# Performance work log

Hardware: AMD Instinct MI355X
Metric: run time of the kernel (lower is better)

The kernel has to match this reference:

```python
import jax, jax.numpy as jnp
import numpy as np

ND, NL, E, M = 8000, 16000, 60000, 50000  # disease nodes, lncrna nodes, edges, label edges
H = 16  # attention heads


def _gat(h_src, h_dst, src, dst, Ws, Wd, a_s, a_d, b, n_dst):
    # PyG GATConv: bipartite, concat heads, add_self_loops=False, negative_slope=0.2
    Hh, C = a_s.shape
    zs = (h_src @ Ws).reshape(-1, Hh, C)   # [Ns,H,C]
    zd = (h_dst @ Wd).reshape(-1, Hh, C)   # [Nd,H,C]
    al = (zs * a_s).sum(-1)[src] + (zd * a_d).sum(-1)[dst]  # [E,H]
    al = jax.nn.leaky_relu(al, negative_slope=0.2)
    m = jax.ops.segment_max(al, dst, num_segments=n_dst)
    m = jnp.where(jnp.isfinite(m), m, 0.0)  # guard empty segments
    e = jnp.exp(al - m[dst])
    s = jax.ops.segment_sum(e, dst, num_segments=n_dst)
    alpha = e / (s[dst] + 1e-16)            # softmax over incoming edges per dst
    msg = zs[src] * alpha[:, :, None]       # [E,H,C]
    out = jax.ops.segment_sum(msg, dst, num_segments=n_dst)
    return out.reshape(n_dst, Hh * C) + b


def _head_mean(x):
    x = jax.nn.relu(x)
    return x.reshape(x.shape[0], H, -1).mean(axis=1)


def _forward(x_d, x_l, emb_d, emb_l, lin_dw, lin_db, lin_lw, lin_lb,
             Wsrc1, Wdst1, asrc1, adst1, b1,
             Wsrc2, Wdst2, asrc2, adst2, b2,
             Wsrc3, Wdst3, asrc3, adst3, b3,
             pw, pb, fc1w, fc1b, fc2w, fc2b,
             node_id_d, node_id_l, edge_src, edge_dst, label_src, label_dst):
    hd = x_d @ lin_dw + lin_db + emb_d[node_id_d]   # [ND,128]
    hl = x_l @ lin_lw + lin_lb + emb_l[node_id_l]   # [NL,128]
    for (Ws, Wd, a_s, a_d, b) in ((Wsrc1, Wdst1, asrc1, adst1, b1),
                                  (Wsrc2, Wdst2, asrc2, adst2, b2),
                                  (Wsrc3, Wdst3, asrc3, adst3, b3)):
        # to_hetero: edge-type 0 = disease->lncrna (target lncrna); 1 = reverse
        out_l = _gat(hd, hl, edge_src, edge_dst, Ws[0], Wd[0], a_s[0], a_d[0], b[0], NL)
        out_d = _gat(hl, hd, edge_dst, edge_src, Ws[1], Wd[1], a_s[1], a_d[1], b[1], ND)
        hd, hl = _head_mean(out_d), _head_mean(out_l)
    # penalty scaling (per node type after to_hetero); transformer branch is dead code
    hd = hd * jnp.exp(hd @ pw[0] + pb[0])
    hl = hl * jnp.exp(hl @ pw[1] + pb[1])
    f = jnp.concatenate([hd[label_src], hl[label_dst]], axis=-1)  # [M,64]
    return jax.nn.relu(f @ fc1w + fc1b) @ fc2w + fc2b              # [M,1]


def setup_inputs():
    key = jax.random.key(0)
    ks = jax.random.split(key, 40)
    def rn(i, shape, scale=1.0):
        return jax.random.normal(ks[i], shape, dtype=jnp.float32) * scale
    return dict(
        x_d=rn(0, (ND, 412)), x_l=rn(1, (NL, 240)),
        node_id_d=jnp.arange(ND), node_id_l=jnp.arange(NL),
        edge_src=jax.random.randint(ks[2], (E,), 0, ND),
        edge_dst=jax.random.randint(ks[3], (E,), 0, NL),
        label_src=jax.random.randint(ks[4], (M,), 0, ND),
        label_dst=jax.random.randint(ks[5], (M,), 0, NL),
        emb_d=rn(6, (ND, 128), 0.1), emb_l=rn(7, (NL, 128), 0.1),
        lin_dw=rn(8, (412, 128), 412 ** -0.5), lin_db=rn(9, (128,), 0.02),
        lin_lw=rn(10, (240, 128), 240 ** -0.5), lin_lb=rn(11, (128,), 0.02),
        Wsrc1=rn(12, (2, 128, 2048), 128 ** -0.5), Wdst1=rn(13, (2, 128, 2048), 128 ** -0.5),
        asrc1=rn(14, (2, H, 128), 0.05), adst1=rn(15, (2, H, 128), 0.05), b1=rn(16, (2, 2048), 0.02),
        Wsrc2=rn(17, (2, 128, 2048), 128 ** -0.5), Wdst2=rn(18, (2, 128, 2048), 128 ** -0.5),
        asrc2=rn(19, (2, H, 128), 0.05), adst2=rn(20, (2, H, 128), 0.05), b2=rn(21, (2, 2048), 0.02),
        Wsrc3=rn(22, (2, 128, 512), 128 ** -0.5), Wdst3=rn(23, (2, 128, 512), 128 ** -0.5),
        asrc3=rn(24, (2, H, 32), 0.05), adst3=rn(25, (2, H, 32), 0.05), b3=rn(26, (2, 512), 0.02),
        pw=rn(27, (2, 32, 1), 0.05), pb=rn(28, (2, 1), 0.01),
        fc1w=rn(29, (64, 64), 64 ** -0.5), fc1b=rn(30, (64,), 0.02),
        fc2w=rn(31, (64, 1), 64 ** -0.5), fc2b=rn(32, (1,), 0.02),
    )


def reference(x_d, x_l, node_id_d, node_id_l, edge_src, edge_dst, label_src, label_dst,
              emb_d, emb_l, lin_dw, lin_db, lin_lw, lin_lb,
              Wsrc1, Wdst1, asrc1, adst1, b1,
              Wsrc2, Wdst2, asrc2, adst2, b2,
              Wsrc3, Wdst3, asrc3, adst3, b3,
              pw, pb, fc1w, fc1b, fc2w, fc2b):
    return _forward(x_d, x_l, emb_d, emb_l, lin_dw, lin_db, lin_lw, lin_lb,
                    Wsrc1, Wdst1, asrc1, adst1, b1,
                    Wsrc2, Wdst2, asrc2, adst2, b2,
                    Wsrc3, Wdst3, asrc3, adst3, b3,
                    pw, pb, fc1w, fc1b, fc2w, fc2b,
                    node_id_d, node_id_l, edge_src, edge_dst, label_src, label_dst)
```

## Files before the change

### kernel.cpp

```cpp
#include <hip/hip_runtime.h>
#include <cstdint>
#include <cstddef>

#define ND 8000
#define NL 16000
#define NE 60000
#define NM 50000

#define BM 64
#define BN 64
#define BK 16

typedef __attribute__((ext_vector_type(8))) short bf16x8;
typedef __attribute__((ext_vector_type(4))) float f32x4;
typedef __attribute__((ext_vector_type(8))) unsigned int u32x8;

__device__ __forceinline__ unsigned short f2bf(float x) {
    unsigned int u = __float_as_uint(x);
    unsigned int r = (u + 0x7FFFu + ((u >> 16) & 1u)) >> 16;
    return (unsigned short)r;
}
__device__ __forceinline__ float bf2f(unsigned short b) {
    return __uint_as_float(((unsigned int)b) << 16);
}
__device__ __forceinline__ float lrelu(float x) {
    return x >= 0.f ? x : 0.2f * x;
}

__device__ __forceinline__ void gl_lds16(const void* g, void* l) {
    __builtin_amdgcn_global_load_lds(
        (const __attribute__((address_space(1))) void*)g,
        (__attribute__((address_space(3))) void*)l, 16, 0, 0);
}

__global__ __launch_bounds__(256) void gemm3_kernel(
    const float* __restrict__ hd, const float* __restrict__ hl,
    const float* __restrict__ W,
    float* __restrict__ zs3d, float* __restrict__ zs3l)
{
    __shared__ float As[BK][BM + 4];
    __shared__ float Bs[BK][BN + 4];
    int mt = blockIdx.y;
    const float* A; const float* B; float* Cm;
    if (mt < 125) { A = hd; B = W; Cm = zs3d; }
    else { mt -= 125; A = hl; B = W + 128 * 512; Cm = zs3l; }
    const int tid = threadIdx.x;
    const int tx = tid & 15, ty = tid >> 4;
    const int bm = mt * BM, bn = blockIdx.x * BN;
    float acc[4][4] = {};
    for (int k0 = 0; k0 < 128; k0 += BK) {
#pragma unroll
        for (int i = 0; i < 4; ++i) {
            int idx = tid + i * 256;
            int ml = idx >> 4, kl = idx & 15;
            As[kl][ml] = A[(size_t)(bm + ml) * 128 + k0 + kl];
        }
#pragma unroll
        for (int i = 0; i < 4; ++i) {
            int idx = tid + i * 256;
            int kl = idx >> 6, nl = idx & 63;
            Bs[kl][nl] = B[(size_t)(k0 + kl) * 512 + bn + nl];
        }
        __syncthreads();
#pragma unroll
        for (int k = 0; k < BK; ++k) {
            float4 av = *(const float4*)&As[k][ty * 4];
            float4 bv = *(const float4*)&Bs[k][tx * 4];
            float a4[4] = {av.x, av.y, av.z, av.w};
            float b4[4] = {bv.x, bv.y, bv.z, bv.w};
#pragma unroll
            for (int i = 0; i < 4; ++i)
#pragma unroll
                for (int j = 0; j < 4; ++j)
                    acc[i][j] += a4[i] * b4[j];
        }
        __syncthreads();
    }
#pragma unroll
    for (int i = 0; i < 4; ++i) {
        int gm = bm + ty * 4 + i;
        int gn0 = bn + tx * 4;
        float4 v;
        float* vp = &v.x;
#pragma unroll
        for (int j = 0; j < 4; ++j) vp[j] = acc[i][j];
        *(float4*)&Cm[(size_t)gm * 512 + gn0] = v;
    }
}

__global__ __launch_bounds__(256) void inlin_kernel(
    const float* __restrict__ x_d, const float* __restrict__ x_l,
    const float* __restrict__ wd, const float* __restrict__ wl,
    const float* __restrict__ bd, const float* __restrict__ bl,
    const float* __restrict__ embd, const float* __restrict__ embl,
    const int* __restrict__ nidd, const int* __restrict__ nidl,
    float* __restrict__ hd, float* __restrict__ hl)
{
    __shared__ float As[BK][32 + 4];
    __shared__ float Bs[BK][BN + 4];
    int mt = blockIdx.y;
    const float* A; const float* B; const float* bias; const float* emb;
    const int* nid; float* out;
    int K;
    if (mt < 250) {
        A = x_d; B = wd; bias = bd; emb = embd; nid = nidd; out = hd; K = 412;
    } else {
        mt -= 250;
        A = x_l; B = wl; bias = bl; emb = embl; nid = nidl; out = hl; K = 240;
    }
    const int tid = threadIdx.x;
    const int tx = tid & 15, ty = tid >> 4;
    const int bm = mt * 32, bn = blockIdx.x * BN;

    const int aml0 = tid >> 4, akl0 = tid & 15;
    const int aml1 = (tid + 256) >> 4, akl1 = tid & 15;
    const int bkl = tid >> 6, bnl = tid & 63;

    float pa[2], pb[4];
    {
        int gk0 = akl0, gk1 = akl1;
        pa[0] = (gk0 < K) ? A[(size_t)(bm + aml0) * K + gk0] : 0.f;
        pa[1] = (gk1 < K) ? A[(size_t)(bm + aml1) * K + gk1] : 0.f;
#pragma unroll
        for (int i = 0; i < 4; ++i) {
            int gk = bkl + i * 4;
            pb[i] = (gk < K) ? B[(size_t)gk * 128 + bn + bnl] : 0.f;
        }
    }

    float acc[2][4] = {};
    for (int k0 = 0; k0 < K; k0 += BK) {
        As[akl0][aml0] = pa[0];
        As[akl1][aml1] = pa[1];
#pragma unroll
        for (int i = 0; i < 4; ++i)
            Bs[bkl + i * 4][bnl] = pb[i];
        __syncthreads();
        int kn = k0 + BK;
        if (kn < K) {
            int gk0 = kn + akl0, gk1 = kn + akl1;
            pa[0] = (gk0 < K) ? A[(size_t)(bm + aml0) * K + gk0] : 0.f;
            pa[1] = (gk1 < K) ? A[(size_t)(bm + aml1) * K + gk1] : 0.f;
#pragma unroll
            for (int i = 0; i < 4; ++i) {
                int gk = kn + bkl + i * 4;
                pb[i] = (gk < K) ? B[(size_t)gk * 128 + bn + bnl] : 0.f;
            }
        }
#pragma unroll
        for (int k = 0; k < BK; ++k) {
            float a0 = As[k][ty * 2];
            float a1 = As[k][ty * 2 + 1];
            float4 bv = *(const float4*)&Bs[k][tx * 4];
            float b4[4] = {bv.x, bv.y, bv.z, bv.w};
#pragma unroll
            for (int j = 0; j < 4; ++j) {
                acc[0][j] += a0 * b4[j];
                acc[1][j] += a1 * b4[j];
            }
        }
        __syncthreads();
    }
#pragma unroll
    for (int i = 0; i < 2; ++i) {
        int gm = bm + ty * 2 + i;
        int gn0 = bn + tx * 4;
        const float* ep = emb + (size_t)nid[gm] * 128 + gn0;
        float4 v;
        float* vp = &v.x;
#pragma unroll
        for (int j = 0; j < 4; ++j)
            vp[j] = acc[i][j] + bias[gn0 + j] + ep[j];
        *(float4*)&out[(size_t)gm * 128 + gn0] = v;
    }
}

__global__ void wt2_kernel(const float* __restrict__ W0, const float* __restrict__ W1,
                           unsigned short* __restrict__ WtH, unsigned short* __restrict__ WtL)
{
    int gid = blockIdx.x * 256 + threadIdx.x;
    if (gid >= 2 * 2 * 128 * 2048) return;
    int l = gid >> 19;
    int rem0 = gid & 524287;
    int dir = rem0 >> 18;
    int rem = rem0 & 262143;
    int k = rem >> 11, n = rem & 2047;
    const float* W = l ? W1 : W0;
    float v = W[(size_t)dir * 262144 + (size_t)k * 2048 + n];
    unsigned short hb = f2bf(v);
    unsigned short lb = f2bf(v - bf2f(hb));
    int u = n >> 4;
    int lane = (n & 15) + 16 * ((k >> 3) & 3);
    size_t o = (size_t)l * 524288 + (size_t)dir * 262144 +
               ((size_t)u * 4 + (k >> 5)) * 512 + lane * 8 + (k & 7);
    WtH[o] = hb;
    WtL[o] = lb;
}

__global__ __launch_bounds__(256) void gemm2r_kernel(
    const unsigned int* __restrict__ haggP,
    const unsigned short* __restrict__ WtH, const unsigned short* __restrict__ WtL,
    const float* __restrict__ bias, float* __restrict__ out, int M)
{
    __shared__ unsigned short BsH[2][8192];
    __shared__ unsigned short BsL[2][8192];

    const int tid = threadIdx.x;
    const int wave = tid >> 6;
    const int lane = tid & 63;
    const int i = blockIdx.x;
    const int cb = i & 1;
    const int mt = i >> 1;
    const int m0 = mt * 64 + wave * 16;
    const int t = m0 >> 4;
    const int row = lane & 15;
    const int quad = lane >> 4;

    const unsigned short* gHb = WtH + (size_t)cb * 8192;
    const unsigned short* gLb = WtL + (size_t)cb * 8192;

    u32x8 pA[4];

    f32x4 mean[4] = {};

#pragma unroll
    for (int j = 0; j < 4; ++j) {
        int o = (tid + j * 256) * 16;
        gl_lds16((const char*)gHb + o, (char*)&BsH[0][0] + o);
        gl_lds16((const char*)gLb + o, (char*)&BsL[0][0] + o);
    }
#pragma unroll
    for (int kc = 0; kc < 4; ++kc)
        pA[kc] = *(const u32x8*)(haggP + (((size_t)t * 16 + 0) * 4 + kc) * 512 + lane * 8);
    __syncthreads();

    int buf = 0;
    for (int h = 0; h < 16; ++h) {
        bf16x8 aH[4], aL[4];
#pragma unroll
        for (int kc = 0; kc < 4; ++kc) {
#pragma unroll
            for (int ii = 0; ii < 8; ++ii) {
                aH[kc][ii] = (short)(pA[kc][ii] & 0xffffu);
                aL[kc][ii] = (short)(pA[kc][ii] >> 16);
            }
        }
        if (h < 15) {
            const char* gH = (const char*)(gHb + (size_t)(h + 1) * 16384);
            const char* gL = (const char*)(gLb + (size_t)(h + 1) * 16384);
            char* lH = (char*)&BsH[buf ^ 1][0];
            char* lL = (char*)&BsL[buf ^ 1][0];
#pragma unroll
            for (int j = 0; j < 4; ++j) {
                int o = (tid + j * 256) * 16;
                gl_lds16(gH + o, lH + o);
                gl_lds16(gL + o, lL + o);
            }
#pragma unroll
            for (int kc = 0; kc < 4; ++kc)
                pA[kc] = *(const u32x8*)(haggP + (((size_t)t * 16 + h + 1) * 4 + kc) * 512 + lane * 8);
        }

#pragma unroll
        for (int ctl = 0; ctl < 4; ++ctl) {
            float bv = bias[h * 128 + cb * 64 + ctl * 16 + row];
            f32x4 accH = (f32x4){bv, bv, bv, bv};
            f32x4 accL = (f32x4){0.f, 0.f, 0.f, 0.f};
#pragma unroll
            for (int kc = 0; kc < 4; ++kc) {
                bf16x8 bH = *(const bf16x8*)&BsH[buf][(ctl * 4 + kc) * 512 + lane * 8];
                bf16x8 bL = *(const bf16x8*)&BsL[buf][(ctl * 4 + kc) * 512 + lane * 8];
                accH = __builtin_amdgcn_mfma_f32_16x16x32_bf16(aH[kc], bH, accH, 0, 0, 0);
                accL = __builtin_amdgcn_mfma_f32_16x16x32_bf16(aH[kc], bL, accL, 0, 0, 0);
                accL = __builtin_amdgcn_mfma_f32_16x16x32_bf16(aL[kc], bH, accL, 0, 0, 0);
            }
#pragma unroll
            for (int r = 0; r < 4; ++r)
                mean[ctl][r] += fmaxf(accH[r] + accL[r], 0.f);
        }
        __syncthreads();
        buf ^= 1;
    }

#pragma unroll
    for (int ctl = 0; ctl < 4; ++ctl) {
        int c = cb * 64 + ctl * 16 + row;
#pragma unroll
        for (int r = 0; r < 4; ++r) {
            int gm = m0 + quad * 4 + r;
            out[(size_t)gm * 128 + c] = mean[ctl][r] * (1.f / 16.f);
        }
    }
}

__global__ void fold3_kernel(
    const float* __restrict__ Ws1, const float* __restrict__ Wd1,
    const float* __restrict__ as1, const float* __restrict__ ad1,
    const float* __restrict__ Ws2, const float* __restrict__ Wd2,
    const float* __restrict__ as2, const float* __restrict__ ad2,
    const float* __restrict__ Ws3, const float* __restrict__ Wd3,
    const float* __restrict__ as3, const float* __restrict__ ad3,
    float* __restrict__ fw3)
{
    int gid = blockIdx.x * blockDim.x + threadIdx.x;
    if (gid >= 3 * 4 * 128 * 16) return;
    int l = gid / 8192, rem1 = gid % 8192;
    int f = rem1 / 2048, rem = rem1 % 2048;
    int k = rem >> 4, h = rem & 15;
    int Ntot = (l == 2) ? 512 : 2048;
    int C = Ntot >> 4;
    const float* W;
    const float* a;
    if (l == 0) { W = (f & 1) ? Wd1 : Ws1; a = (f & 1) ? ad1 : as1; }
    else if (l == 1) { W = (f & 1) ? Wd2 : Ws2; a = (f & 1) ? ad2 : as2; }
    else { W = (f & 1) ? Wd3 : Ws3; a = (f & 1) ? ad3 : as3; }
    if (f >= 2) { W += 128 * Ntot; a += 16 * C; }
    float s = 0.f;
    for (int c = 0; c < C; ++c) s += W[(size_t)k * Ntot + h * C + c] * a[h * C + c];
    fw3[gid] = s;
}

__global__ __launch_bounds__(256) void score2both_kernel(
    const float* __restrict__ Hd, const float* __restrict__ Hl,
    const float* __restrict__ fw,
    float* __restrict__ ssb0, float* __restrict__ sdb1,
    float* __restrict__ sdb0, float* __restrict__ ssb1)
{
    __shared__ float hs[16 * 128];
    __shared__ float wa[128 * 16];
    __shared__ float wb[128 * 16];
    int b = blockIdx.x;
    const float* Hf; const float* WfA; const float* WfB;
    float* outA; float* outB; int n0;
    if (b < ND / 16) {
        Hf = Hd; WfA = fw; WfB = fw + 3 * 2048; outA = ssb0; outB = sdb1; n0 = b * 16;
    } else {
        Hf = Hl; WfA = fw + 1 * 2048; WfB = fw + 2 * 2048; outA = sdb0; outB = ssb1;
        n0 = (b - ND / 16) * 16;
    }
    int tid = threadIdx.x;
#pragma unroll
    for (int i = 0; i < 8; ++i) {
        int idx = tid + i * 256;
        int nl = idx >> 7, k = idx & 127;
        hs[idx] = Hf[(size_t)(n0 + nl) * 128 + k];
        wa[idx] = WfA[idx];
        wb[idx] = WfB[idx];
    }
    __syncthreads();
    int nl = tid >> 4, h = tid & 15;
    float sa = 0.f, sb = 0.f;
    for (int k = 0; k < 128; ++k) {
        float hv = hs[nl * 128 + k];
        sa += hv * wa[k * 16 + h];
        sb += hv * wb[k * 16 + h];
    }
    int gn = n0 + nl;
    outA[gn * 16 + h] = sa;
    outB[gn * 16 + h] = sb;
}

__global__ void ms_kernel(
    const int* __restrict__ esrc, const int* __restrict__ edst,
    const float* __restrict__ ssb0, const float* __restrict__ sdb0,
    const float* __restrict__ ssb1, const float* __restrict__ sdb1,
    const int* __restrict__ offl, const int* __restrict__ csrl, float* __restrict__ msl,
    const int* __restrict__ offd, const int* __restrict__ csrd, float* __restrict__ msd)
{
    int t = blockIdx.x * 256 + threadIdx.x;
    const int* off; const int* csr; const int* srcidx;
    const float* ss; float sdv; float* ms; int d, h;
    if (t < NL * 16) {
        d = t >> 4; h = t & 15;
        off = offl; csr = csrl; srcidx = esrc; ss = ssb0;
        sdv = sdb0[d * 16 + h]; ms = msl;
    } else {
        t -= NL * 16;
        if (t >= ND * 16) return;
        d = t >> 4; h = t & 15;
        off = offd; csr = csrd; srcidx = edst; ss = ssb1;
        sdv = sdb1[d * 16 + h]; ms = msd;
    }
    int e0 = off[d], e1 = off[d + 1];
    float m = -1e30f, s = 0.f;
    for (int e = e0; e < e1; ++e) {
        int sn = srcidx[csr[e]];
        float a = lrelu(ss[sn * 16 + h] + sdv);
        if (a > m) { s = s * __expf(m - a) + 1.f; m = a; }
        else s += __expf(a - m);
    }
    ms[d * 32 + h] = m;
    ms[d * 32 + 16 + h] = s + 1e-16f;
}

__global__ void hist_kernel(const int* __restrict__ esrc, const int* __restrict__ edst,
                            int* __restrict__ degl, int* __restrict__ degd)
{
    int e = blockIdx.x * blockDim.x + threadIdx.x;
    if (e >= NE) return;
    atomicAdd(&degl[edst[e]], 1);
    atomicAdd(&degd[esrc[e]], 1);
}

__global__ __launch_bounds__(1024) void scan2_kernel(
    const int* __restrict__ degA, int* __restrict__ offA, int nA,
    const int* __restrict__ degB, int* __restrict__ offB, int nB)
{
    __shared__ int ps[1024];
    const int* deg = blockIdx.x ? degB : degA;
    int* off = blockIdx.x ? offB : offA;
    int n = blockIdx.x ? nB : nA;
    int tid = threadIdx.x;
    int chunk = (n + 1023) >> 10;
    int start = tid * chunk, end = min(start + chunk, n);
    int p = 0;
    for (int i = start; i < end; ++i) p += deg[i];
    ps[tid] = p;
    __syncthreads();
    for (int o = 1; o < 1024; o <<= 1) {
        int v = (tid >= o) ? ps[tid - o] : 0;
        __syncthreads();
        ps[tid] += v;
        __syncthreads();
    }
    int run = ps[tid] - p;
    for (int i = start; i < end; ++i) { off[i] = run; run += deg[i]; }
    if (tid == 1023) off[n] = ps[1023];
}

__global__ void scatter_kernel(const int* __restrict__ esrc, const int* __restrict__ edst,
                               const int* __restrict__ offl, const int* __restrict__ offd,
                               int* __restrict__ curl, int* __restrict__ curd,
                               int* __restrict__ csrl, int* __restrict__ csrd)
{
    int e = blockIdx.x * blockDim.x + threadIdx.x;
    if (e >= NE) return;
    int dl = edst[e]; int p = atomicAdd(&curl[dl], 1); csrl[offl[dl] + p] = e;
    int dd = esrc[e]; int q = atomicAdd(&curd[dd], 1); csrd[offd[dd] + q] = e;
}

__global__ __launch_bounds__(256) void hagg_kernel(
    const float* __restrict__ hsrc,
    const float* __restrict__ ss,
    const float* __restrict__ sd,
    const float* __restrict__ ms,
    const int* __restrict__ off, const int* __restrict__ csr, const int* __restrict__ srcidx,
    unsigned int* __restrict__ haggP)
{
    __shared__ float alpha_s[2][8][17];
    __shared__ int src_s[2][8];
    const int d0 = blockIdx.x * 2;
    const int tid = threadIdx.x;

    const int half = tid >> 7;
    const int c = tid & 127;
    const int d = d0 + half;
    const int my_e0 = off[d];
    const int my_deg = off[d + 1] - my_e0;
    const int deg0 = off[d0 + 1] - off[d0];
    const int deg1 = off[d0 + 2] - off[d0 + 1];
    const int degmax = deg0 > deg1 ? deg0 : deg1;
    const int ntrip = (degmax + 7) >> 3;

    float acc[16];
#pragma unroll
    for (int h = 0; h < 16; ++h) acc[h] = 0.f;

    for (int trip = 0; trip < ntrip; ++trip) {
        int ce = trip * 8;
        {
            int ei = c >> 4, h = c & 15;
            if (ce + ei < my_deg) {
                int eid = csr[my_e0 + ce + ei];
                int sn = srcidx[eid];
                float a = lrelu(ss[sn * 16 + h] + sd[d * 16 + h]);
                alpha_s[half][ei][h] = __expf(a - ms[d * 32 + h]) / ms[d * 32 + 16 + h];
                if (h == 0) src_s[half][ei] = sn;
            }
        }
        __syncthreads();
        int nc = min(8, my_deg - ce);
        for (int ei = 0; ei < nc; ++ei) {
            float v = hsrc[(size_t)src_s[half][ei] * 128 + c];
#pragma unroll
            for (int h = 0; h < 16; ++h)
                acc[h] += alpha_s[half][ei][h] * v;
        }
        __syncthreads();
    }

    const int t = d >> 4;
    const int lane8 = ((d & 15) + 16 * ((c >> 3) & 3)) * 8 + (c & 7);
    const int kc = c >> 5;
#pragma unroll
    for (int h = 0; h < 16; ++h) {
        float v = acc[h];
        unsigned short hb = f2bf(v);
        unsigned short lb = f2bf(v - bf2f(hb));
        size_t idx = (((size_t)t * 16 + h) * 4 + kc) * 512 + lane8;
        haggP[idx] = (unsigned int)hb | ((unsigned int)lb << 16);
    }
}

__global__ __launch_bounds__(256) void agg32both_kernel(
    const float* __restrict__ zs3d, const float* __restrict__ zs3l,
    const float* __restrict__ ssb0, const float* __restrict__ sdb0, const float* __restrict__ msl,
    const float* __restrict__ ssb1, const float* __restrict__ sdb1, const float* __restrict__ msd,
    const int* __restrict__ offl, const int* __restrict__ csrl,
    const int* __restrict__ offd, const int* __restrict__ csrd,
    const int* __restrict__ esrc, const int* __restrict__ edst,
    const float* __restrict__ bias512,
    const float* __restrict__ pw, const float* __restrict__ pb,
    float* __restrict__ hlp, float* __restrict__ hdp)
{
    __shared__ float alpha_s[16][17];
    __shared__ int src_s[16];
    __shared__ float lds_out[512];
    __shared__ float hrow[32];
    int d = blockIdx.x;
    const float* zs; const float* ss; const float* sd; const float* ms;
    const int* off; const int* csr; const int* srcidx;
    const float* bias; const float* pwt; const float* pbt; float* out;
    if (d < NL) {
        zs = zs3d; ss = ssb0; sd = sdb0; ms = msl;
        off = offl; csr = csrl; srcidx = esrc;
        bias = bias512; pwt = pw + 32; pbt = pb + 1; out = hlp;
    } else {
        d -= NL;
        zs = zs3l; ss = ssb1; sd = sdb1; ms = msd;
        off = offd; csr = csrd; srcidx = edst;
        bias = bias512 + 512; pwt = pw; pbt = pb; out = hdp;
    }
    const int tid = threadIdx.x;
    const int e0 = off[d], e1 = off[d + 1];

    float acc0 = 0.f, acc1 = 0.f;
    const int hsel = tid >> 4;

    for (int ce = e0; ce < e1; ce += 16) {
        int nc = min(16, e1 - ce);
        if (tid < nc * 16) {
            int ei = tid >> 4, h = tid & 15;
            int eid = csr[ce + ei];
            int sn = srcidx[eid];
            float a = lrelu(ss[sn * 16 + h] + sd[d * 16 + h]);
            alpha_s[ei][h] = __expf(a - ms[d * 32 + h]) / ms[d * 32 + 16 + h];
            if (h == 0) src_s[ei] = sn;
        }
        __syncthreads();
        for (int ei = 0; ei < nc; ++ei) {
            float a = alpha_s[ei][hsel];
            float2 v = *(const float2*)(zs + (size_t)src_s[ei] * 512 + tid * 2);
            acc0 += a * v.x;
            acc1 += a * v.y;
        }
        __syncthreads();
    }

    lds_out[tid * 2] = fmaxf(acc0 + bias[tid * 2], 0.f);
    lds_out[tid * 2 + 1] = fmaxf(acc1 + bias[tid * 2 + 1], 0.f);
    __syncthreads();
    if (tid < 32) {
        float s = 0.f;
#pragma unroll
        for (int hh = 0; hh < 16; ++hh) s += lds_out[hh * 32 + tid];
        hrow[tid] = s * (1.f / 16.f);
    }
    __syncthreads();
    if (tid < 32) {
        float t = pbt[0];
#pragma unroll
        for (int c = 0; c < 32; ++c) t += hrow[c] * pwt[c];
        out[(size_t)d * 32 + tid] = hrow[tid] * expf(t);
    }
}

__global__ __launch_bounds__(256) void mlp_kernel(
    const float* __restrict__ hd, const float* __restrict__ hl,
    const int* __restrict__ ls, const int* __restrict__ ld,
    const float* __restrict__ w1, const float* __restrict__ b1,
    const float* __restrict__ w2, const float* __restrict__ b2,
    float* __restrict__ out, int M)
{
    __shared__ float w1s[64 * 64];
    __shared__ float b1s[64];
    __shared__ float w2s[64];
    int tid = threadIdx.x;
#pragma unroll
    for (int i = 0; i < 16; ++i) w1s[tid + i * 256] = w1[tid + i * 256];
    if (tid < 64) { b1s[tid] = b1[tid]; w2s[tid] = w2[tid]; }
    __syncthreads();
    int m = blockIdx.x * 256 + tid;
    if (m >= M) return;
    float f[64];
    const float* hp = hd + (size_t)ls[m] * 32;
    const float* lp = hl + (size_t)ld[m] * 32;
#pragma unroll
    for (int c = 0; c < 32; ++c) { f[c] = hp[c]; f[32 + c] = lp[c]; }
    float o = b2[0];
    for (int j = 0; j < 64; ++j) {
        float hj = b1s[j];
#pragma unroll
        for (int k = 0; k < 64; ++k) hj += f[k] * w1s[k * 64 + j];
        hj = fmaxf(hj, 0.f);
        o += hj * w2s[j];
    }
    out[m] = o;
}

extern "C" void kernel_launch(void* const* d_in, const int* in_sizes, int n_in,
                              void* d_out, int out_size, void* d_ws, size_t ws_size,
                              hipStream_t stream)
{
    const float* x_d = (const float*)d_in[0];
    const float* x_l = (const float*)d_in[1];
    const int* node_id_d = (const int*)d_in[2];
    const int* node_id_l = (const int*)d_in[3];
    const int* edge_src = (const int*)d_in[4];
    const int* edge_dst = (const int*)d_in[5];
    const int* label_src = (const int*)d_in[6];
    const int* label_dst = (const int*)d_in[7];
    const float* emb_d = (const float*)d_in[8];
    const float* emb_l = (const float*)d_in[9];
    const float* lin_dw = (const float*)d_in[10];
    const float* lin_db = (const float*)d_in[11];
    const float* lin_lw = (const float*)d_in[12];
    const float* lin_lb = (const float*)d_in[13];
    const float* Ws[3] = {(const float*)d_in[14], (const float*)d_in[19], (const float*)d_in[24]};
    const float* Wd[3] = {(const float*)d_in[15], (const float*)d_in[20], (const float*)d_in[25]};
    const float* as_[3] = {(const float*)d_in[16], (const float*)d_in[21], (const float*)d_in[26]};
    const float* ad_[3] = {(const float*)d_in[17], (const float*)d_in[22], (const float*)d_in[27]};
    const float* bb[3] = {(const float*)d_in[18], (const float*)d_in[23], (const float*)d_in[28]};
    const float* pw = (const float*)d_in[29];
    const float* pb = (const float*)d_in[30];
    const float* fc1w = (const float*)d_in[31];
    const float* fc1b = (const float*)d_in[32];
    const float* fc2w = (const float*)d_in[33];
    const float* fc2b = (const float*)d_in[34];

    char* wsb = (char*)d_ws;
    size_t woff = 0;
    auto carve = [&](size_t bytes) -> void* {
        woff = (woff + 255) & ~(size_t)255;
        void* p = wsb + woff;
        woff += bytes;
        return p;
    };
    float* hdA = (float*)carve((size_t)ND * 128 * 4);
    float* hlA = (float*)carve((size_t)NL * 128 * 4);
    float* hdB = (float*)carve((size_t)ND * 128 * 4);
    float* hlB = (float*)carve((size_t)NL * 128 * 4);
    unsigned int* haggP = (unsigned int*)carve((size_t)NL * 2048 * 4);
    unsigned short* WtH = (unsigned short*)carve((size_t)2 * 2 * 2048 * 128 * 2);
    unsigned short* WtL = (unsigned short*)carve((size_t)2 * 2 * 2048 * 128 * 2);
    float* ssb0 = (float*)carve((size_t)ND * 16 * 4);
    float* sdb0 = (float*)carve((size_t)NL * 16 * 4);
    float* ssb1 = (float*)carve((size_t)NL * 16 * 4);
    float* sdb1 = (float*)carve((size_t)ND * 16 * 4);
    float* msl = (float*)carve((size_t)NL * 32 * 4);
    float* msd = (float*)carve((size_t)ND * 32 * 4);
    float* fw3 = (float*)carve((size_t)3 * 4 * 2048 * 4);
    int* degl = (int*)carve((size_t)(2 * (NL + ND)) * 4);
    int* degd = degl + NL;
    int* curl = degd + ND;
    int* curd = curl + NL;
    int* offl = (int*)carve((size_t)(NL + 1) * 4);
    int* offd = (int*)carve((size_t)(ND + 1) * 4);
    int* csrl = (int*)carve((size_t)NE * 4);
    int* csrd = (int*)carve((size_t)NE * 4);
    float* hdp = (float*)carve((size_t)ND * 32 * 4);
    float* hlp = (float*)carve((size_t)NL * 32 * 4);

    hipMemsetAsync(degl, 0, (size_t)2 * (NL + ND) * 4, stream);

    hist_kernel<<<(NE + 255) / 256, 256, 0, stream>>>(edge_src, edge_dst, degl, degd);
    scan2_kernel<<<2, 1024, 0, stream>>>(degl, offl, NL, degd, offd, ND);
    scatter_kernel<<<(NE + 255) / 256, 256, 0, stream>>>(edge_src, edge_dst, offl, offd, curl, curd, csrl, csrd);

    fold3_kernel<<<(3 * 8192 + 255) / 256, 256, 0, stream>>>(
        Ws[0], Wd[0], as_[0], ad_[0], Ws[1], Wd[1], as_[1], ad_[1],
        Ws[2], Wd[2], as_[2], ad_[2], fw3);
    wt2_kernel<<<(2 * 524288 + 255) / 256, 256, 0, stream>>>(Ws[0], Ws[1], WtH, WtL);

    inlin_kernel<<<dim3(2, 750), 256, 0, stream>>>(
        x_d, x_l, lin_dw, lin_lw, lin_db, lin_lb, emb_d, emb_l,
        node_id_d, node_id_l, hdA, hlA);

    float* hd_cur = hdA; float* hd_nxt = hdB;
    float* hl_cur = hlA; float* hl_nxt = hlB;

    const int grid_ms = ((NL + ND) * 16 + 255) / 256;
    const int gridNL = (NL / 64) * 2;
    const int gridND = (ND / 64) * 2;

    for (int L = 0; L < 2; ++L) {
        const float* fw = fw3 + (size_t)L * 8192;
        const unsigned short* wtH = WtH + (size_t)L * 524288;
        const unsigned short* wtL = WtL + (size_t)L * 524288;

        score2both_kernel<<<ND / 16 + NL / 16, 256, 0, stream>>>(
            hd_cur, hl_cur, fw, ssb0, sdb1, sdb0, ssb1);
        ms_kernel<<<grid_ms, 256, 0, stream>>>(edge_src, edge_dst, ssb0, sdb0, ssb1, sdb1,
                                               offl, csrl, msl, offd, csrd, msd);

        hagg_kernel<<<NL / 2, 256, 0, stream>>>(hd_cur, ssb0, sdb0, msl, offl, csrl, edge_src, haggP);
        gemm2r_kernel<<<gridNL, 256, 0, stream>>>(haggP, wtH, wtL, bb[L], hl_nxt, NL);

        hagg_kernel<<<ND / 2, 256, 0, stream>>>(hl_cur, ssb1, sdb1, msd, offd, csrd, edge_dst, haggP);
        gemm2r_kernel<<<gridND, 256, 0, stream>>>(haggP,
                                                  wtH + (size_t)2048 * 128, wtL + (size_t)2048 * 128,
                                                  bb[L] + 2048, hd_nxt, ND);

        float* t;
        t = hd_cur; hd_cur = hd_nxt; hd_nxt = t;
        t = hl_cur; hl_cur = hl_nxt; hl_nxt = t;
    }

    {
        const float* fw = fw3 + 2 * 8192;
        float* zs3d = (float*)haggP;
        float* zs3l = (float*)haggP + (size_t)ND * 512;
        score2both_kernel<<<ND / 16 + NL / 16, 256, 0, stream>>>(
            hd_cur, hl_cur, fw, ssb0, sdb1, sdb0, ssb1);
        ms_kernel<<<grid_ms, 256, 0, stream>>>(edge_src, edge_dst, ssb0, sdb0, ssb1, sdb1,
                                               offl, csrl, msl, offd, csrd, msd);

        gemm3_kernel<<<dim3(512 / BN, 125 + 250), 256, 0, stream>>>(
            hd_cur, hl_cur, Ws[2], zs3d, zs3l);

        agg32both_kernel<<<NL + ND, 256, 0, stream>>>(
            zs3d, zs3l, ssb0, sdb0, msl, ssb1, sdb1, msd,
            offl, csrl, offd, csrd, edge_src, edge_dst,
            bb[2], pw, pb, hlp, hdp);
    }

    mlp_kernel<<<(NM + 255) / 256, 256, 0, stream>>>(hdp, hlp, label_src, label_dst,
                                                     fc1w, fc1b, fc2w, fc2b, (float*)d_out, NM);
}
```

Baseline: 711.2 us.

## Map one wavefront per destination node in layer-3 aggregation with shuffle reductions

The layer-3 GAT aggregation kernel now packs four destination nodes per 256-thread block, with one 64-lane wavefront per node. Each lane computes its own head's attention coefficient and accumulates 8 contiguous channels through float4 loads. The head-mean and penalty dot product use cross-lane shuffles, which removes the shared-memory staging and block barriers. Each lane recomputes the exp per edge (4 lanes per head share the same value), and there is no batching of edge index loads.

```diff
diff --git a/kernel.cpp b/kernel.cpp
--- a/kernel.cpp
+++ b/kernel.cpp
@@ -513,11 +513,10 @@
     const float* __restrict__ pw, const float* __restrict__ pb,
     float* __restrict__ hlp, float* __restrict__ hdp)
 {
-    __shared__ float alpha_s[16][17];
-    __shared__ int src_s[16];
-    __shared__ float lds_out[512];
-    __shared__ float hrow[32];
-    int d = blockIdx.x;
+    int d = blockIdx.x * 4 + (threadIdx.x >> 6);
+    if (d >= NL + ND) return;
+    const int lane = threadIdx.x & 63;
+
     const float* zs; const float* ss; const float* sd; const float* ms;
     const int* off; const int* csr; const int* srcidx;
     const float* bias; const float* pwt; const float* pbt; float* out;
@@ -531,47 +530,55 @@
         off = offd; csr = csrd; srcidx = edst;
         bias = bias512 + 512; pwt = pw; pbt = pb; out = hdp;
     }
-    const int tid = threadIdx.x;
+
+    const int h = lane >> 2;
+    const int c0 = lane * 8;
+
+    const float sdv = sd[d * 16 + h];
+    const float mh = ms[d * 32 + h];
+    const float sh = ms[d * 32 + 16 + h];
     const int e0 = off[d], e1 = off[d + 1];
 
-    float acc0 = 0.f, acc1 = 0.f;
-    const int hsel = tid >> 4;
-
-    for (int ce = e0; ce < e1; ce += 16) {
-        int nc = min(16, e1 - ce);
-        if (tid < nc * 16) {
-            int ei = tid >> 4, h = tid & 15;
-            int eid = csr[ce + ei];
-            int sn = srcidx[eid];
-            float a = lrelu(ss[sn * 16 + h] + sd[d * 16 + h]);
-            alpha_s[ei][h] = __expf(a - ms[d * 32 + h]) / ms[d * 32 + 16 + h];
-            if (h == 0) src_s[ei] = sn;
-        }
-        __syncthreads();
-        for (int ei = 0; ei < nc; ++ei) {
-            float a = alpha_s[ei][hsel];
-            float2 v = *(const float2*)(zs + (size_t)src_s[ei] * 512 + tid * 2);
-            acc0 += a * v.x;
-            acc1 += a * v.y;
-        }
-        __syncthreads();
-    }
-
-    lds_out[tid * 2] = fmaxf(acc0 + bias[tid * 2], 0.f);
-    lds_out[tid * 2 + 1] = fmaxf(acc1 + bias[tid * 2 + 1], 0.f);
-    __syncthreads();
-    if (tid < 32) {
-        float s = 0.f;
-#pragma unroll
-        for (int hh = 0; hh < 16; ++hh) s += lds_out[hh * 32 + tid];
-        hrow[tid] = s * (1.f / 16.f);
-    }
-    __syncthreads();
-    if (tid < 32) {
-        float t = pbt[0];
-#pragma unroll
-        for (int c = 0; c < 32; ++c) t += hrow[c] * pwt[c];
-        out[(size_t)d * 32 + tid] = hrow[tid] * expf(t);
+    float acc[8] = {};
+    for (int e = e0; e < e1; ++e) {
+        int sn = srcidx[csr[e]];
+        float a = lrelu(ss[sn * 16 + h] + sdv);
+        float alpha = __expf(a - mh) / sh;
+        const float* zr = zs + (size_t)sn * 512 + c0;
+        float4 v0 = *(const float4*)zr;
+        float4 v1 = *(const float4*)(zr + 4);
+        acc[0] += alpha * v0.x; acc[1] += alpha * v0.y;
+        acc[2] += alpha * v0.z; acc[3] += alpha * v0.w;
+        acc[4] += alpha * v1.x; acc[5] += alpha * v1.y;
+        acc[6] += alpha * v1.z; acc[7] += alpha * v1.w;
+    }
+
+#pragma unroll
+    for (int i = 0; i < 8; ++i)
+        acc[i] = fmaxf(acc[i] + bias[c0 + i], 0.f);
+
+#pragma unroll
+    for (int m = 4; m <= 32; m <<= 1)
+#pragma unroll
+        for (int i = 0; i < 8; ++i)
+            acc[i] += __shfl_xor(acc[i], m);
+
+    float hr[8];
+#pragma unroll
+    for (int i = 0; i < 8; ++i) hr[i] = acc[i] * (1.f / 16.f);
+
+    float p = 0.f;
+    const int ko = (lane & 3) * 8;
+#pragma unroll
+    for (int i = 0; i < 8; ++i) p += hr[i] * pwt[ko + i];
+    p += __shfl_xor(p, 1);
+    p += __shfl_xor(p, 2);
+    float t = expf(p + pbt[0]);
+
+    if (lane < 4) {
+        float* op = out + (size_t)d * 32 + lane * 8;
+#pragma unroll
+        for (int i = 0; i < 8; ++i) op[i] = hr[i] * t;
     }
 }
 
@@ -728,7 +735,7 @@
         gemm3_kernel<<<dim3(512 / BN, 125 + 250), 256, 0, stream>>>(
             hd_cur, hl_cur, Ws[2], zs3d, zs3l);
 
-        agg32both_kernel<<<NL + ND, 256, 0, stream>>>(
+        agg32both_kernel<<<(NL + ND) / 4, 256, 0, stream>>>(
             zs3d, zs3l, ssb0, sdb0, msl, ssb1, sdb1, msd,
             offl, csrl, offd, csrd, edge_src, edge_dst,
             bb[2], pw, pb, hlp, hdp);
```

New measurement: 694.1 us. 2.4% less time.
